# Optimization experiments

Measured on AMD Instinct MI355X. Metric: run time of the kernel, lower is better.

Reference implementation:

```python
import jax, jax.numpy as jnp
import numpy as np

NEG_INF = -1000000000.0
B, S, E, H = 2, 2048, 1024, 16
HD = E // H


def setup_inputs() -> dict:
    key = jax.random.key(0)
    ks = jax.random.split(key, 5)
    sd = 1.0 / np.sqrt(E)
    return {
        "x": jax.random.normal(ks[0], (B, S, E), dtype=jnp.float32),
        "Wqkv": jax.random.normal(ks[1], (3 * E, E), dtype=jnp.float32) * sd,
        "bqkv": jax.random.normal(ks[2], (3 * E,), dtype=jnp.float32) * sd,
        "Wout": jax.random.normal(ks[3], (E, E), dtype=jnp.float32) * sd,
        "bout": jax.random.normal(ks[4], (E,), dtype=jnp.float32) * sd,
    }


def reference(x, Wqkv, bqkv, Wout, bout):
    # qkv projection (torch Linear: x @ W.T + b)
    qkv = x @ Wqkv.T + bqkv                      # [B, S, 3E]
    qkv = qkv.reshape(B, S, H, 3 * HD).transpose(0, 2, 1, 3)  # [B, H, S, 3*hd]
    q, k, v = jnp.split(qkv, 3, axis=-1)          # each [B, H, S, hd]
    scaled = jnp.einsum('bhqd,bhkd->bhqk', q, k) / jnp.sqrt(jnp.float32(HD))
    # faithful to source: mask = tril(ones) * NEG_INF (lower triangle incl. diagonal gets -1e9)
    mask = jnp.tril(jnp.ones((S, S), dtype=jnp.float32)) * NEG_INF
    scaled = scaled + mask                        # broadcast over [B, H]
    attention = jax.nn.softmax(scaled, axis=-1)
    values = jnp.einsum('bhqk,bhkd->bhqd', attention, v)
    values = values.transpose(0, 2, 1, 3).reshape(B, S, E)
    out = values @ Wout.T + bout
    return out
```

## Files before the change

### kernel.cpp

```cpp
#include <hip/hip_runtime.h>
#include <hip/hip_bf16.h>
#include <math.h>

#define Bb 2
#define Ss 2048
#define Ee 1024
#define Hh 16
#define HDd 64
#define NEG_INF_F -1000000000.0f

typedef __attribute__((ext_vector_type(8))) short bfrag;
typedef __attribute__((ext_vector_type(4))) float ffrag;
typedef __attribute__((ext_vector_type(16))) float ffrag16;
typedef __attribute__((ext_vector_type(8))) unsigned short us8;

#define C1F 0.1803368801f

__device__ __forceinline__ unsigned short f2bf(float x) {
  unsigned u = __float_as_uint(x);
  u += 0x7fffu + ((u >> 16) & 1u);
  return (unsigned short)(u >> 16);
}
__device__ __forceinline__ float bf2f(unsigned short h) {
  return __uint_as_float(((unsigned)h) << 16);
}

__device__ __forceinline__ void async_copy16(void* lds, const void* g) {
  __builtin_amdgcn_global_load_lds(
      (const __attribute__((address_space(1))) unsigned int*)g,
      (__attribute__((address_space(3))) unsigned int*)lds, 16, 0, 0);
}

__global__ __launch_bounds__(256) void split_all(
    const float* __restrict__ x, unsigned short* __restrict__ xh,
    const float* __restrict__ wq, unsigned short* __restrict__ wqh,
    unsigned short* __restrict__ wql,
    const float* __restrict__ wo, unsigned short* __restrict__ woh,
    unsigned short* __restrict__ wol) {
  int bid = blockIdx.x;
  const float* in;
  unsigned short *hi, *lo;
  if (bid < 4096) { in = x; hi = xh; lo = nullptr; }
  else if (bid < 7168) { bid -= 4096; in = wq; hi = wqh; lo = wql; }
  else { bid -= 7168; in = wo; hi = woh; lo = wol; }
  const int idx = (bid * 256 + threadIdx.x) * 4;
  const float4 v = *(const float4*)(in + idx);
  unsigned short h0 = f2bf(v.x), h1 = f2bf(v.y), h2 = f2bf(v.z), h3 = f2bf(v.w);
  ushort4 hv = {h0, h1, h2, h3};
  *(ushort4*)(hi + idx) = hv;
  if (lo) {
    ushort4 lv = {f2bf(v.x - bf2f(h0)), f2bf(v.y - bf2f(h1)),
                  f2bf(v.z - bf2f(h2)), f2bf(v.w - bf2f(h3))};
    *(ushort4*)(lo + idx) = lv;
  }
}

__device__ __forceinline__ int gemm_slot(int row, int q) {
  return (row >> 1) * 8 + ((((row & 1) * 4) | q) ^ ((row >> 1) & 7));
}
__device__ __forceinline__ int slot_src_off(int slot, int ld) {
  const int dr = slot >> 3;
  const int idx8 = (slot & 7) ^ (dr & 7);
  const int row = dr * 2 + (idx8 >> 2);
  const int q = idx8 & 3;
  return row * ld + q * 8;
}

__global__ __launch_bounds__(256) void gemm_qkv(
    const unsigned short* __restrict__ Ah,
    const unsigned short* __restrict__ Bh, const unsigned short* __restrict__ Bl,
    const float* __restrict__ bias,
    unsigned short* __restrict__ q_h,
    unsigned short* __restrict__ k_h, unsigned short* __restrict__ k_l,
    unsigned short* __restrict__ vt_h) {
  __shared__ unsigned short sm[3 * 4096];
  const int tid = threadIdx.x;
  const int lane = tid & 63;
  const int w = tid >> 6;
  const int wm = w >> 1;
  const int wn = w & 1;
  const int l31 = lane & 31;
  const int e = lane >> 5;
  const int m0 = blockIdx.x * 128;
  const int n0 = blockIdx.y * 128;

  int coff[2], ldsb[2];
#pragma unroll
  for (int u = 0; u < 2; ++u) {
    const int slot = w * 128 + u * 64 + lane;
    coff[u] = slot_src_off(slot, 1024);
    ldsb[u] = (w * 128 + u * 64) * 8;
  }
  const unsigned short* srcs[3] = {
      Ah + (size_t)m0 * 1024, Bh + (size_t)n0 * 1024, Bl + (size_t)n0 * 1024};

  ffrag16 acc[2][2];
#pragma unroll
  for (int i = 0; i < 2; ++i)
#pragma unroll
    for (int j = 0; j < 2; ++j) acc[i][j] = (ffrag16)0.f;

  int ca[2][2], cb[2][2];
#pragma unroll
  for (int t = 0; t < 2; ++t)
#pragma unroll
    for (int h2 = 0; h2 < 2; ++h2) {
      ca[t][h2] = gemm_slot(wm * 64 + t * 32 + l31, h2 * 2 + e) * 8;
      cb[t][h2] = gemm_slot(wn * 64 + t * 32 + l31, h2 * 2 + e) * 8;
    }

  for (int k0 = 0; k0 < 1024; k0 += 32) {
    __syncthreads();
#pragma unroll
    for (int t = 0; t < 3; ++t)
#pragma unroll
      for (int u = 0; u < 2; ++u)
        async_copy16(&sm[t * 4096 + ldsb[u]], srcs[t] + coff[u] + k0);
    __syncthreads();

    bfrag ah[2][2], bhf[2][2], blf[2][2];
#pragma unroll
    for (int t = 0; t < 2; ++t)
#pragma unroll
      for (int h2 = 0; h2 < 2; ++h2) {
        ah[t][h2] = *(const bfrag*)&sm[0 * 4096 + ca[t][h2]];
        bhf[t][h2] = *(const bfrag*)&sm[1 * 4096 + cb[t][h2]];
        blf[t][h2] = *(const bfrag*)&sm[2 * 4096 + cb[t][h2]];
      }
#pragma unroll
    for (int mt = 0; mt < 2; ++mt)
#pragma unroll
      for (int nt = 0; nt < 2; ++nt)
#pragma unroll
        for (int h2 = 0; h2 < 2; ++h2) {
          acc[mt][nt] = __builtin_amdgcn_mfma_f32_32x32x16_bf16(
              ah[mt][h2], bhf[nt][h2], acc[mt][nt], 0, 0, 0);
          acc[mt][nt] = __builtin_amdgcn_mfma_f32_32x32x16_bf16(
              ah[mt][h2], blf[nt][h2], acc[mt][nt], 0, 0, 0);
        }
  }

#pragma unroll
  for (int nt = 0; nt < 2; ++nt) {
    const int n = n0 + wn * 64 + nt * 32 + l31;
    const float bv = bias[n];
    const int h = n / 192;
    const int c = n - h * 192;
    const int d = c & 63;
#pragma unroll
    for (int mt = 0; mt < 2; ++mt) {
      if (c >= 128) {
#pragma unroll
        for (int g = 0; g < 4; ++g) {
          const int m = m0 + wm * 64 + mt * 32 + g * 8 + e * 4;
          const int bidx = m >> 11;
          const int s = m & 2047;
          ushort4 hv4;
          unsigned short* ph = (unsigned short*)&hv4;
#pragma unroll
          for (int r = 0; r < 4; ++r)
            ph[r] = f2bf(acc[mt][nt][g * 4 + r] + bv);
          const size_t off =
              (size_t)(bidx * 16 + h) * (64 * 2048) + (size_t)d * 2048 + s;
          *(ushort4*)(vt_h + off) = hv4;
        }
      } else if (c < 64) {
#pragma unroll
        for (int g = 0; g < 4; ++g)
#pragma unroll
          for (int r = 0; r < 4; ++r) {
            const int m = m0 + wm * 64 + mt * 32 + g * 8 + e * 4 + r;
            const int bidx = m >> 11;
            const int s = m & 2047;
            const size_t off =
                (size_t)(bidx * 16 + h) * (2048 * 64) + (size_t)s * 64 + d;
            q_h[off] = f2bf((acc[mt][nt][g * 4 + r] + bv) * C1F);
          }
      } else {
#pragma unroll
        for (int g = 0; g < 4; ++g)
#pragma unroll
          for (int r = 0; r < 4; ++r) {
            const int m = m0 + wm * 64 + mt * 32 + g * 8 + e * 4 + r;
            const int bidx = m >> 11;
            const int s = m & 2047;
            const float val = acc[mt][nt][g * 4 + r] + bv;
            const unsigned short hv = f2bf(val);
            const size_t off =
                (size_t)(bidx * 16 + h) * (2048 * 64) + (size_t)s * 64 + d;
            k_h[off] = hv;
            k_l[off] = f2bf(val - bf2f(hv));
          }
      }
    }
  }
}

__global__ __launch_bounds__(256) void gemm_out2(
    const unsigned short* __restrict__ A,
    const unsigned short* __restrict__ Bh, const unsigned short* __restrict__ Bl,
    const float* __restrict__ bias, float* __restrict__ out) {
  __shared__ unsigned short sm[8192];
  const int tid = threadIdx.x;
  const int lane = tid & 63;
  const int w = tid >> 6;
  const int wm = w >> 1;
  const int wn = w & 1;
  const int l31 = lane & 31;
  const int e = lane >> 5;
  const int m0 = blockIdx.x * 128;
  const int n0 = blockIdx.y * 64;

  int acoff[2], aldsb[2];
#pragma unroll
  for (int u = 0; u < 2; ++u) {
    const int slot = w * 128 + u * 64 + lane;
    acoff[u] = slot_src_off(slot, 1024);
    aldsb[u] = (w * 128 + u * 64) * 8;
  }
  const int bslot = w * 64 + lane;
  const int bcoff = slot_src_off(bslot, 1024);
  const int bldsb = bslot * 8;

  const unsigned short* Ap  = A + (size_t)m0 * 1024;
  const unsigned short* Bph = Bh + (size_t)n0 * 1024;
  const unsigned short* Bpl = Bl + (size_t)n0 * 1024;

  ffrag16 acc[2];
  acc[0] = (ffrag16)0.f;
  acc[1] = (ffrag16)0.f;

  int ca[2][2], cb[2];
#pragma unroll
  for (int t = 0; t < 2; ++t)
#pragma unroll
    for (int h2 = 0; h2 < 2; ++h2)
      ca[t][h2] = gemm_slot(wm * 64 + t * 32 + l31, h2 * 2 + e) * 8;
#pragma unroll
  for (int h2 = 0; h2 < 2; ++h2)
    cb[h2] = gemm_slot(wn * 32 + l31, h2 * 2 + e) * 8;

  for (int k0 = 0; k0 < 1024; k0 += 32) {
    __syncthreads();
#pragma unroll
    for (int u = 0; u < 2; ++u)
      async_copy16(&sm[0 + aldsb[u]], Ap + acoff[u] + k0);
    async_copy16(&sm[4096 + bldsb], Bph + bcoff + k0);
    async_copy16(&sm[6144 + bldsb], Bpl + bcoff + k0);
    __syncthreads();

    bfrag ah[2][2], bhf[2], blf[2];
#pragma unroll
    for (int t = 0; t < 2; ++t)
#pragma unroll
      for (int h2 = 0; h2 < 2; ++h2)
        ah[t][h2] = *(const bfrag*)&sm[0 + ca[t][h2]];
#pragma unroll
    for (int h2 = 0; h2 < 2; ++h2) {
      bhf[h2] = *(const bfrag*)&sm[4096 + cb[h2]];
      blf[h2] = *(const bfrag*)&sm[6144 + cb[h2]];
    }
#pragma unroll
    for (int mt = 0; mt < 2; ++mt)
#pragma unroll
      for (int h2 = 0; h2 < 2; ++h2) {
        acc[mt] = __builtin_amdgcn_mfma_f32_32x32x16_bf16(
            ah[mt][h2], bhf[h2], acc[mt], 0, 0, 0);
        acc[mt] = __builtin_amdgcn_mfma_f32_32x32x16_bf16(
            ah[mt][h2], blf[h2], acc[mt], 0, 0, 0);
      }
  }

  const int n = n0 + wn * 32 + l31;
  const float bv = bias[n];
#pragma unroll
  for (int mt = 0; mt < 2; ++mt)
#pragma unroll
    for (int g = 0; g < 4; ++g)
#pragma unroll
      for (int r = 0; r < 4; ++r) {
        const int m = m0 + wm * 64 + mt * 32 + g * 8 + e * 4 + r;
        out[(size_t)m * 1024 + n] = acc[mt][g * 4 + r] + bv;
      }
}

__global__ __launch_bounds__(256) void attn_ks(
    const unsigned short* __restrict__ qh,
    const unsigned short* __restrict__ kh, const unsigned short* __restrict__ kl,
    const unsigned short* __restrict__ vth,
    unsigned short* __restrict__ pO, float* __restrict__ pl) {
  __shared__ unsigned short sm[12288 + 8192];
  const int tid = threadIdx.x;
  const int lane = tid & 63;
  const int w = tid >> 6;
  const int l15 = lane & 15;
  const int quad = lane >> 4;
  const int bh = blockIdx.x;
  const int y = blockIdx.y;
  const int z = blockIdx.z;
  const int rbase[2] = {64 * y + 16 * w, 64 * (31 - y) + 16 * w};
  const int ktB = 31 - y;
  const int E0 = (y <= 7) ? (y + 17) : 24;
  const int kts = z ? E0 : y;
  const int kte = z ? 32 : E0;
  const bool fix = (y == 0) && (w == 3);
  const size_t base = (size_t)bh * (Ss * HDd);
  const int PB = 12288;

  bfrag Qh[2][2];
#pragma unroll
  for (int mt = 0; mt < 2; ++mt)
#pragma unroll
    for (int ks = 0; ks < 2; ++ks) {
      const size_t off = base + (size_t)(rbase[mt] + l15) * 64 + ks * 32 + quad * 8;
      Qh[mt][ks] = *(const bfrag*)(qh + off);
    }

  bfrag vone;
#pragma unroll
  for (int j = 0; j < 8; ++j) vone[j] = (short)0x3F80;

  const int c0 = w * 128 + lane;
  const int c1 = c0 + 64;
  const int r0 = c0 >> 3, r1 = c1 >> 3;
  const int s0 = ((c0 & 7) ^ (r0 & 7)) * 8;
  const int s1 = ((c1 & 7) ^ (r1 & 7)) * 8;
  const int koff0 = r0 * 64 + s0, koff1 = r1 * 64 + s1;
  const int voff0 = r0 * 2048 + s0, voff1 = r1 * 2048 + s1;
  const int ldsc0 = (w * 128) * 8;
  const int ldsc1 = (w * 128 + 64) * 8;

  ffrag O[2][4], Oe[2], Vsum[4];
#pragma unroll
  for (int mt = 0; mt < 2; ++mt) {
#pragma unroll
    for (int dt = 0; dt < 4; ++dt) O[mt][dt] = (ffrag)0.f;
    Oe[mt] = (ffrag)0.f;
  }
#pragma unroll
  for (int dt = 0; dt < 4; ++dt) Vsum[dt] = (ffrag)0.f;

  for (int kt = kts; kt < kte; ++kt) {
    const unsigned short* kph = kh + base + kt * 4096;
    const unsigned short* kpl = kl + base + kt * 4096;
    const unsigned short* vph = vth + base + kt * 64;
    __syncthreads();
    async_copy16(&sm[0 + ldsc0], kph + koff0);
    async_copy16(&sm[0 + ldsc1], kph + koff1);
    async_copy16(&sm[4096 + ldsc0], kpl + koff0);
    async_copy16(&sm[4096 + ldsc1], kpl + koff1);
    async_copy16(&sm[8192 + ldsc0], vph + voff0);
    async_copy16(&sm[8192 + ldsc1], vph + voff1);
    __syncthreads();

    const bool bact = (kt >= ktB);

    ffrag S[2][4];
#pragma unroll
    for (int mt = 0; mt < 2; ++mt)
#pragma unroll
      for (int nt = 0; nt < 4; ++nt) S[mt][nt] = (ffrag)0.f;
#pragma unroll
    for (int nt = 0; nt < 4; ++nt) {
      const int krow = nt * 16 + l15;
#pragma unroll
      for (int ks = 0; ks < 2; ++ks) {
        const int koffr = krow * 64 + ((ks * 4 + quad) ^ (krow & 7)) * 8;
        const bfrag kbh = *(const bfrag*)&sm[koffr];
        const bfrag kbl = *(const bfrag*)&sm[4096 + koffr];
        S[0][nt] = __builtin_amdgcn_mfma_f32_16x16x32_bf16(Qh[0][ks], kbh, S[0][nt], 0, 0, 0);
        S[0][nt] = __builtin_amdgcn_mfma_f32_16x16x32_bf16(Qh[0][ks], kbl, S[0][nt], 0, 0, 0);
        if (bact) {
          S[1][nt] = __builtin_amdgcn_mfma_f32_16x16x32_bf16(Qh[1][ks], kbh, S[1][nt], 0, 0, 0);
          S[1][nt] = __builtin_amdgcn_mfma_f32_16x16x32_bf16(Qh[1][ks], kbl, S[1][nt], 0, 0, 0);
        }
      }
    }

    const float CM = -1.442695041e9f;
#pragma unroll
    for (int mt = 0; mt < 2; ++mt) {
      if (mt == 1 && !bact) continue;
      const bool partial = (kt == (mt == 0 ? y : ktB));
#pragma unroll
      for (int nt = 0; nt < 4; ++nt) {
        const int key = nt * 16 + l15;
#pragma unroll
        for (int rp = 0; rp < 2; ++rp) {
          float t0 = S[mt][nt][2 * rp];
          float t1 = S[mt][nt][2 * rp + 1];
          if (partial) {
            const int jg = kt * 64 + key;
            const int ig = rbase[mt] + quad * 4 + 2 * rp;
            if (jg <= ig) t0 += CM;
            if (jg <= ig + 1) t1 += CM;
          }
          float2 pf;
          pf.x = __builtin_amdgcn_exp2f(t0);
          pf.y = __builtin_amdgcn_exp2f(t1);
          const __hip_bfloat162 pb = __float22bfloat162_rn(pf);
          const unsigned short* pbs = (const unsigned short*)&pb;
          const int prow0 = w * 32 + mt * 16 + quad * 4 + 2 * rp;
          sm[PB + prow0 * 64 + (((key >> 3) ^ (prow0 & 7)) * 8 + (key & 7))] = pbs[0];
          const int prow1 = prow0 + 1;
          sm[PB + prow1 * 64 + (((key >> 3) ^ (prow1 & 7)) * 8 + (key & 7))] = pbs[1];
        }
      }
    }

#pragma unroll
    for (int ks = 0; ks < 2; ++ks) {
      bfrag pA[2];
#pragma unroll
      for (int mt = 0; mt < 2; ++mt) {
        if (mt == 1 && !bact) continue;
        const int prow = w * 32 + mt * 16 + l15;
        pA[mt] = *(const bfrag*)&sm[PB + prow * 64 + ((ks * 4 + quad) ^ (prow & 7)) * 8];
      }
      Oe[0] = __builtin_amdgcn_mfma_f32_16x16x32_bf16(pA[0], vone, Oe[0], 0, 0, 0);
      if (bact)
        Oe[1] = __builtin_amdgcn_mfma_f32_16x16x32_bf16(pA[1], vone, Oe[1], 0, 0, 0);
#pragma unroll
      for (int dt = 0; dt < 4; ++dt) {
        const int vrow = dt * 16 + l15;
        const int voffr = 8192 + vrow * 64 + ((ks * 4 + quad) ^ (vrow & 7)) * 8;
        const bfrag vbh = *(const bfrag*)&sm[voffr];
        O[0][dt] = __builtin_amdgcn_mfma_f32_16x16x32_bf16(pA[0], vbh, O[0][dt], 0, 0, 0);
        if (bact)
          O[1][dt] = __builtin_amdgcn_mfma_f32_16x16x32_bf16(pA[1], vbh, O[1][dt], 0, 0, 0);
        if (fix)
          Vsum[dt] = __builtin_amdgcn_mfma_f32_16x16x32_bf16(vone, vbh, Vsum[dt], 0, 0, 0);
      }
    }
  }

  const size_t pbase = (size_t)z * (32 * 2048 * 64) + (size_t)bh * (2048 * 64);
  const int lbase = z * 65536 + bh * 2048;
  const float lfix = 64.0f * (float)(kte - kts);
#pragma unroll
  for (int mt = 0; mt < 2; ++mt)
#pragma unroll
    for (int r = 0; r < 4; ++r) {
      const int s = rbase[mt] + quad * 4 + r;
      const bool fl = fix && mt == 1 && quad == 3 && r == 3;
#pragma unroll
      for (int dt = 0; dt < 4; ++dt) {
        const float val = fl ? Vsum[dt][r] : O[mt][dt][r];
        pO[pbase + (size_t)s * 64 + dt * 16 + l15] = f2bf(val);
      }
      if (l15 == 0) pl[lbase + s] = fl ? lfix : Oe[mt][r];
    }
}

__global__ __launch_bounds__(256) void merge_vals(
    const unsigned short* __restrict__ pO, const float* __restrict__ pl,
    unsigned short* __restrict__ vals) {
  const int idx = (blockIdx.x * 256 + threadIdx.x) * 4;
  const int d = idx & 63;
  const int sbh = idx >> 6;
  const int s = sbh & 2047;
  const int bh = sbh >> 11;
  const size_t zstr = (size_t)32 * 2048 * 64;
  const ushort4 o0 = *(const ushort4*)(pO + (size_t)sbh * 64 + d);
  const ushort4 o1 = *(const ushort4*)(pO + zstr + (size_t)sbh * 64 + d);
  const float inv = 1.0f / (pl[sbh] + pl[65536 + sbh]);
  ushort4 rv;
  rv.x = f2bf((bf2f(o0.x) + bf2f(o1.x)) * inv);
  rv.y = f2bf((bf2f(o0.y) + bf2f(o1.y)) * inv);
  rv.z = f2bf((bf2f(o0.z) + bf2f(o1.z)) * inv);
  rv.w = f2bf((bf2f(o0.w) + bf2f(o1.w)) * inv);
  const int b = bh >> 4;
  const int h = bh & 15;
  *(ushort4*)(vals + ((size_t)b * 2048 + s) * 1024 + h * 64 + d) = rv;
}

extern "C" void kernel_launch(void* const* d_in, const int* in_sizes, int n_in,
                              void* d_out, int out_size, void* d_ws, size_t ws_size,
                              hipStream_t stream) {
  const float* x    = (const float*)d_in[0];
  const float* Wqkv = (const float*)d_in[1];
  const float* bqkv = (const float*)d_in[2];
  const float* Wout = (const float*)d_in[3];
  const float* bout = (const float*)d_in[4];
  float* out = (float*)d_out;
  char* wsb = (char*)d_ws;

  unsigned short* qhp  = (unsigned short*)d_ws;
  unsigned short* khp  = qhp + 1 * 4194304;
  unsigned short* klp  = qhp + 2 * 4194304;
  unsigned short* vthp = qhp + 3 * 4194304;
  unsigned short* vals = qhp + 4 * 4194304;
  unsigned short* pO   = (unsigned short*)(wsb + (40u << 20));
  float*          pl   = (float*)(wsb + (56u << 20));
  unsigned short* wqh  = (unsigned short*)(wsb + (48u << 20));
  unsigned short* wql  = (unsigned short*)(wsb + (54u << 20));
  unsigned short* woh  = (unsigned short*)(wsb + (60u << 20));
  unsigned short* wol  = (unsigned short*)(wsb + (62u << 20));
  unsigned short* xh   = (unsigned short*)d_out;

  dim3 blk(256);
  split_all<<<8192, blk, 0, stream>>>(x, xh, Wqkv, wqh, wql, Wout, woh, wol);
  gemm_qkv<<<dim3(32, 24), blk, 0, stream>>>(xh, wqh, wql, bqkv,
                                             qhp, khp, klp, vthp);
  attn_ks<<<dim3(32, 16, 2), blk, 0, stream>>>(qhp, khp, klp, vthp, pO, pl);
  merge_vals<<<4096, blk, 0, stream>>>(pO, pl, vals);
  gemm_out2<<<dim3(32, 16), blk, 0, stream>>>(vals, woh, wol, bout, out);
}
```

Baseline: 232.3 us.

## Merge attention query tiles into 512-thread blocks with double-buffered K/V loads

The attention kernel now uses 512-thread blocks, each covering two adjacent query tile pairs, so one K/V tile loaded into shared memory serves eight warps instead of four. K/V loads become double-buffered: the next tile is prefetched asynchronously into the alternate buffer while the current one is computed, which removes one barrier per iteration. Warps whose rows are fully masked for a key tile skip that tile's MFMAs through per-warp activity flags. The key-split boundaries change to match, at the cost of more LDS per block and fewer, larger blocks.

```diff
diff --git a/kernel.cpp b/kernel.cpp
--- a/kernel.cpp
+++ b/kernel.cpp
@@ -284,28 +284,29 @@
       }
 }
 
-__global__ __launch_bounds__(256) void attn_ks(
+__global__ __launch_bounds__(512) void attn_ks8(
     const unsigned short* __restrict__ qh,
     const unsigned short* __restrict__ kh, const unsigned short* __restrict__ kl,
     const unsigned short* __restrict__ vth,
     unsigned short* __restrict__ pO, float* __restrict__ pl) {
-  __shared__ unsigned short sm[12288 + 8192];
+  __shared__ unsigned short sm[2 * 12288 + 16384];
   const int tid = threadIdx.x;
   const int lane = tid & 63;
   const int w = tid >> 6;
+  const int wl = w & 3;
   const int l15 = lane & 15;
   const int quad = lane >> 4;
   const int bh = blockIdx.x;
-  const int y = blockIdx.y;
+  const int j = blockIdx.y;
   const int z = blockIdx.z;
-  const int rbase[2] = {64 * y + 16 * w, 64 * (31 - y) + 16 * w};
-  const int ktB = 31 - y;
-  const int E0 = (y <= 7) ? (y + 17) : 24;
-  const int kts = z ? E0 : y;
-  const int kte = z ? 32 : E0;
-  const bool fix = (y == 0) && (w == 3);
+  const int yw = 2 * j + (w >> 2);
+  const int rbase[2] = {64 * yw + 16 * wl, 64 * (31 - yw) + 16 * wl};
+  const int ktB = 31 - yw;
+  const int kts = z ? (j + 16) : (2 * j);
+  const int kte = z ? 32 : (j + 16);
+  const bool fix = (yw == 0) && (wl == 3);
   const size_t base = (size_t)bh * (Ss * HDd);
-  const int PB = 12288;
+  const int PB = 24576;
 
   bfrag Qh[2][2];
 #pragma unroll
@@ -318,17 +319,14 @@
 
   bfrag vone;
 #pragma unroll
-  for (int j = 0; j < 8; ++j) vone[j] = (short)0x3F80;
-
-  const int c0 = w * 128 + lane;
-  const int c1 = c0 + 64;
-  const int r0 = c0 >> 3, r1 = c1 >> 3;
+  for (int jj = 0; jj < 8; ++jj) vone[jj] = (short)0x3F80;
+
+  const int c0 = w * 64 + lane;
+  const int r0 = c0 >> 3;
   const int s0 = ((c0 & 7) ^ (r0 & 7)) * 8;
-  const int s1 = ((c1 & 7) ^ (r1 & 7)) * 8;
-  const int koff0 = r0 * 64 + s0, koff1 = r1 * 64 + s1;
-  const int voff0 = r0 * 2048 + s0, voff1 = r1 * 2048 + s1;
-  const int ldsc0 = (w * 128) * 8;
-  const int ldsc1 = (w * 128 + 64) * 8;
+  const int koff0 = r0 * 64 + s0;
+  const int voff0 = r0 * 2048 + s0;
+  const int ldsc0 = (w * 64) * 8;
 
   ffrag O[2][4], Oe[2], Vsum[4];
 #pragma unroll
@@ -340,19 +338,22 @@
 #pragma unroll
   for (int dt = 0; dt < 4; ++dt) Vsum[dt] = (ffrag)0.f;
 
+  {
+    async_copy16(&sm[0 + ldsc0], kh + base + kts * 4096 + koff0);
+    async_copy16(&sm[4096 + ldsc0], kl + base + kts * 4096 + koff0);
+    async_copy16(&sm[8192 + ldsc0], vth + base + kts * 64 + voff0);
+  }
+
+  int bufo = 0;
   for (int kt = kts; kt < kte; ++kt) {
-    const unsigned short* kph = kh + base + kt * 4096;
-    const unsigned short* kpl = kl + base + kt * 4096;
-    const unsigned short* vph = vth + base + kt * 64;
     __syncthreads();
-    async_copy16(&sm[0 + ldsc0], kph + koff0);
-    async_copy16(&sm[0 + ldsc1], kph + koff1);
-    async_copy16(&sm[4096 + ldsc0], kpl + koff0);
-    async_copy16(&sm[4096 + ldsc1], kpl + koff1);
-    async_copy16(&sm[8192 + ldsc0], vph + voff0);
-    async_copy16(&sm[8192 + ldsc1], vph + voff1);
-    __syncthreads();
-
+    if (kt + 1 < kte) {
+      const int alt = bufo ^ 12288;
+      async_copy16(&sm[alt + 0 + ldsc0], kh + base + (kt + 1) * 4096 + koff0);
+      async_copy16(&sm[alt + 4096 + ldsc0], kl + base + (kt + 1) * 4096 + koff0);
+      async_copy16(&sm[alt + 8192 + ldsc0], vth + base + (kt + 1) * 64 + voff0);
+    }
+    const bool aact = (kt >= yw);
     const bool bact = (kt >= ktB);
 
     ffrag S[2][4];
@@ -365,11 +366,13 @@
       const int krow = nt * 16 + l15;
 #pragma unroll
       for (int ks = 0; ks < 2; ++ks) {
-        const int koffr = krow * 64 + ((ks * 4 + quad) ^ (krow & 7)) * 8;
+        const int koffr = bufo + krow * 64 + ((ks * 4 + quad) ^ (krow & 7)) * 8;
         const bfrag kbh = *(const bfrag*)&sm[koffr];
         const bfrag kbl = *(const bfrag*)&sm[4096 + koffr];
-        S[0][nt] = __builtin_amdgcn_mfma_f32_16x16x32_bf16(Qh[0][ks], kbh, S[0][nt], 0, 0, 0);
-        S[0][nt] = __builtin_amdgcn_mfma_f32_16x16x32_bf16(Qh[0][ks], kbl, S[0][nt], 0, 0, 0);
+        if (aact) {
+          S[0][nt] = __builtin_amdgcn_mfma_f32_16x16x32_bf16(Qh[0][ks], kbh, S[0][nt], 0, 0, 0);
+          S[0][nt] = __builtin_amdgcn_mfma_f32_16x16x32_bf16(Qh[0][ks], kbl, S[0][nt], 0, 0, 0);
+        }
         if (bact) {
           S[1][nt] = __builtin_amdgcn_mfma_f32_16x16x32_bf16(Qh[1][ks], kbh, S[1][nt], 0, 0, 0);
           S[1][nt] = __builtin_amdgcn_mfma_f32_16x16x32_bf16(Qh[1][ks], kbl, S[1][nt], 0, 0, 0);
@@ -380,8 +383,9 @@
     const float CM = -1.442695041e9f;
 #pragma unroll
     for (int mt = 0; mt < 2; ++mt) {
+      if (mt == 0 && !aact) continue;
       if (mt == 1 && !bact) continue;
-      const bool partial = (kt == (mt == 0 ? y : ktB));
+      const bool partial = (kt == (mt == 0 ? yw : ktB));
 #pragma unroll
       for (int nt = 0; nt < 4; ++nt) {
         const int key = nt * 16 + l15;
@@ -413,25 +417,29 @@
       bfrag pA[2];
 #pragma unroll
       for (int mt = 0; mt < 2; ++mt) {
+        if (mt == 0 && !aact) continue;
         if (mt == 1 && !bact) continue;
         const int prow = w * 32 + mt * 16 + l15;
         pA[mt] = *(const bfrag*)&sm[PB + prow * 64 + ((ks * 4 + quad) ^ (prow & 7)) * 8];
       }
-      Oe[0] = __builtin_amdgcn_mfma_f32_16x16x32_bf16(pA[0], vone, Oe[0], 0, 0, 0);
+      if (aact)
+        Oe[0] = __builtin_amdgcn_mfma_f32_16x16x32_bf16(pA[0], vone, Oe[0], 0, 0, 0);
       if (bact)
         Oe[1] = __builtin_amdgcn_mfma_f32_16x16x32_bf16(pA[1], vone, Oe[1], 0, 0, 0);
 #pragma unroll
       for (int dt = 0; dt < 4; ++dt) {
         const int vrow = dt * 16 + l15;
-        const int voffr = 8192 + vrow * 64 + ((ks * 4 + quad) ^ (vrow & 7)) * 8;
+        const int voffr = bufo + 8192 + vrow * 64 + ((ks * 4 + quad) ^ (vrow & 7)) * 8;
         const bfrag vbh = *(const bfrag*)&sm[voffr];
-        O[0][dt] = __builtin_amdgcn_mfma_f32_16x16x32_bf16(pA[0], vbh, O[0][dt], 0, 0, 0);
+        if (aact)
+          O[0][dt] = __builtin_amdgcn_mfma_f32_16x16x32_bf16(pA[0], vbh, O[0][dt], 0, 0, 0);
         if (bact)
           O[1][dt] = __builtin_amdgcn_mfma_f32_16x16x32_bf16(pA[1], vbh, O[1][dt], 0, 0, 0);
         if (fix)
           Vsum[dt] = __builtin_amdgcn_mfma_f32_16x16x32_bf16(vone, vbh, Vsum[dt], 0, 0, 0);
       }
     }
+    bufo ^= 12288;
   }
 
   const size_t pbase = (size_t)z * (32 * 2048 * 64) + (size_t)bh * (2048 * 64);
@@ -502,7 +510,7 @@
   split_all<<<8192, blk, 0, stream>>>(x, xh, Wqkv, wqh, wql, Wout, woh, wol);
   gemm_qkv<<<dim3(32, 24), blk, 0, stream>>>(xh, wqh, wql, bqkv,
                                              qhp, khp, klp, vthp);
-  attn_ks<<<dim3(32, 16, 2), blk, 0, stream>>>(qhp, khp, klp, vthp, pO, pl);
+  attn_ks8<<<dim3(32, 8, 2), dim3(512), 0, stream>>>(qhp, khp, klp, vthp, pO, pl);
   merge_vals<<<4096, blk, 0, stream>>>(pO, pl, vals);
   gemm_out2<<<dim3(32, 16), blk, 0, stream>>>(vals, woh, wol, bout, out);
 }
```

Result: no change. 229.6 us (-1.2%).
